# Performance work log

Hardware: AMD Instinct MI355X
Metric: run time of the kernel (lower is better)

## Reference

```python
import jax, jax.numpy as jnp
import numpy as np

NUM_HEADS = 12


def setup_inputs() -> dict:
    key = jax.random.key(0)
    ks = jax.random.split(key, 6)
    B, H, W, C = 8, 32, 32, 768
    hd = C // NUM_HEADS
    n = lambda k, shp, sc: jax.random.normal(k, shp, dtype=jnp.float32) * sc
    return {
        "x": n(ks[0], (B, H, W, C), 1.0),
        "qkv_w": n(ks[1], (3 * C, C), 0.02),
        "qkv_b": jnp.zeros((3 * C,), jnp.float32),
        "proj_w": n(ks[2], (C, C), 0.02),
        "proj_b": jnp.zeros((C,), jnp.float32),
        "rel_pos_h": n(ks[3], (2 * H - 1, hd), 0.02),
        "rel_pos_w": n(ks[4], (2 * W - 1, hd), 0.02),
    }


def reference(x, qkv_w, qkv_b, proj_w, proj_b, rel_pos_h, rel_pos_w):
    B, H, W, C = x.shape
    nH = NUM_HEADS
    hd = C // nH
    scale = hd ** -0.5
    # qkv projection (torch Linear convention: y = x @ W.T + b)
    qkv = x.reshape(B, H * W, C) @ qkv_w.T + qkv_b              # (B, HW, 3C)
    qkv = qkv.reshape(B, H * W, 3, nH, hd).transpose(2, 0, 3, 1, 4)
    qkv = qkv.reshape(3, B * nH, H * W, hd)
    q, k, v = qkv[0], qkv[1], qkv[2]
    attn = jnp.einsum('bqd,bkd->bqk', q * scale, k)             # (B*nH, HW, HW)
    # decomposed relative position bias (q_size == k_size, so no interpolation)
    coords_h = jnp.arange(H)[:, None] - jnp.arange(H)[None, :] + (H - 1)
    coords_w = jnp.arange(W)[:, None] - jnp.arange(W)[None, :] + (W - 1)
    Rh = rel_pos_h[coords_h]                                    # (H, H, hd)
    Rw = rel_pos_w[coords_w]                                    # (W, W, hd)
    r_q = q.reshape(B * nH, H, W, hd)
    rel_h = jnp.einsum('bhwc,hkc->bhwk', r_q, Rh)               # (B*nH, H, W, H)
    rel_w = jnp.einsum('bhwc,wkc->bhwk', r_q, Rw)               # (B*nH, H, W, W)
    attn = (attn.reshape(B * nH, H, W, H, W)
            + rel_h[..., :, None] + rel_w[..., None, :]).reshape(B * nH, H * W, H * W)
    attn = jax.nn.softmax(attn, axis=-1)
    out = attn @ v                                              # (B*nH, HW, hd)
    out = out.reshape(B, nH, H, W, hd).transpose(0, 2, 3, 1, 4).reshape(B, H, W, C)
    return out @ proj_w.T + proj_b
```

## Files before the change

### kernel.cpp

```cpp
#include <hip/hip_runtime.h>

using u16 = unsigned short;
using u32 = unsigned int;
typedef __attribute__((ext_vector_type(8))) short bf16x8;
typedef __attribute__((ext_vector_type(4))) float f32x4;

__device__ __forceinline__ float bf2f(u32 h) {
  union { u32 u; float f; } c; c.u = h << 16; return c.f;
}
__device__ __forceinline__ u16 f2bf(float f) {
  union { float f; u32 u; } c; c.f = f;
  u32 u = c.u;
  u32 r = (u + 0x7FFFu + ((u >> 16) & 1u)) >> 16;
  return (u16)r;
}

#define GLD16(gsrc, ldst)                                                      \
  __builtin_amdgcn_global_load_lds(                                            \
      (const __attribute__((address_space(1))) unsigned int*)(gsrc),           \
      (__attribute__((address_space(3))) unsigned int*)(ldst), 16, 0, 0)

__device__ __forceinline__ int kappa(int ss) {
  return (ss & 0x23) | ((ss & 0x10) >> 2) | ((ss & 0x0C) << 1);
}

__device__ __forceinline__ bf16x8 onehot8(int c) {
  union { u32 w[4]; bf16x8 v; } u;
  u32 hv = (c & 1) ? 0x3F800000u : 0x3F80u;
#pragma unroll
  for (int k = 0; k < 4; ++k) u.w[k] = ((c >> 1) == k) ? hv : 0u;
  return u.v;
}

__global__ void cvt_kernel(const float* __restrict__ src, u16* __restrict__ dst, int n) {
  int i = (blockIdx.x * blockDim.x + threadIdx.x) * 4;
  if (i < n) {
    float4 v = *(const float4*)(src + i);
    ushort4 o;
    o.x = f2bf(v.x); o.y = f2bf(v.y); o.z = f2bf(v.z); o.w = f2bf(v.w);
    *(ushort4*)(dst + i) = o;
  }
}

__global__ void tbl_kernel(const float* __restrict__ rph, const float* __restrict__ rpw,
                           u16* __restrict__ tbl) {
  int i = blockIdx.x * 256 + threadIdx.x;
  int row = i >> 6, d = i & 63;
  float v = 0.f;
  if (row < 63) v = rph[row * 64 + d];
  else if (row >= 64 && row < 127) v = rpw[(row - 64) * 64 + d];
  tbl[i] = f2bf(v * 8.0f);
}

__global__ __launch_bounds__(256, 2) void pgemm_kernel(
    const u16* __restrict__ A, const u16* __restrict__ tbl, u16* __restrict__ Q2) {
  __shared__ u16 As[128 * 64];
  __shared__ u16 Bs[128 * 64];
  const int tid = threadIdx.x;
  const int lane = tid & 63, wave = tid >> 6;
  const int lr = lane & 15, lg = lane >> 4;
  const int m0 = blockIdx.x * 128;
  const int wm = (wave >> 1) * 64, wn = (wave & 1) * 64;

#pragma unroll
  for (int i = 0; i < 4; ++i) {
    int c = tid + i * 256;
    int row = c >> 3, pp = c & 7;
    int pl = pp ^ (row & 7);
    GLD16(A + (size_t)(m0 + row) * 128 + pl * 8, &As[c * 8]);
    GLD16(tbl + row * 64 + pl * 8, &Bs[c * 8]);
  }
  __syncthreads();

  bf16x8 a[4][2], b[4][2];
#pragma unroll
  for (int m = 0; m < 4; ++m) {
    int row = wm + m * 16 + lr;
#pragma unroll
    for (int kf = 0; kf < 2; ++kf)
      a[m][kf] = *(const bf16x8*)&As[(row * 64 + kf * 32 + lg * 8) ^ ((row & 7) << 3)];
  }
#pragma unroll
  for (int n = 0; n < 4; ++n) {
    int row = wn + n * 16 + lr;
#pragma unroll
    for (int kf = 0; kf < 2; ++kf)
      b[n][kf] = *(const bf16x8*)&Bs[(row * 64 + kf * 32 + lg * 8) ^ ((row & 7) << 3)];
  }

  f32x4 acc[4][4] = {};
#pragma unroll
  for (int kf = 0; kf < 2; ++kf)
#pragma unroll
    for (int m = 0; m < 4; ++m)
#pragma unroll
      for (int n = 0; n < 4; ++n)
        acc[m][n] = __builtin_amdgcn_mfma_f32_16x16x32_bf16(a[m][kf], b[n][kf], acc[m][n], 0, 0, 0);

#pragma unroll
  for (int m = 0; m < 4; ++m)
#pragma unroll
    for (int n = 0; n < 4; ++n) {
      const int col = wn + n * 16 + lr;
#pragma unroll
      for (int r = 0; r < 4; ++r) {
        const int g = m0 + wm + m * 16 + lg * 4 + r;
        const int s = g & 1023;
        const int hq = s >> 5, w = s & 31;
        u16 hv = f2bf(acc[m][n][r]);
        if (col < 64) {
          int kh = hq + 31 - col;
          if ((unsigned)kh < 32u) Q2[(size_t)g * 128 + 96 + kh] = hv;
        } else {
          int kw = w + 95 - col;
          if ((unsigned)kw < 32u) Q2[(size_t)g * 128 + 64 + kw] = hv;
        }
      }
    }
}

template <int MODE>
__global__ __launch_bounds__(512, 2) void gemm128(
    const u16* __restrict__ A, const u16* __restrict__ B,
    const float* __restrict__ bias, u16* __restrict__ oq, u16* __restrict__ ok,
    u16* __restrict__ ovt, float* __restrict__ ofp) {
  __shared__ u16 As[2][128 * 64];
  __shared__ u16 Bs[2][128 * 64];
  const int tid = threadIdx.x;
  const int lane = tid & 63, wave = tid >> 6;
  const int lr = lane & 15, lg = lane >> 4;

  const int nbx = (MODE == 0) ? 18 : 6;
  const int nwg = nbx * 64;
  int id = blockIdx.y * nbx + blockIdx.x;
  int nid = (id & 7) * (nwg >> 3) + (id >> 3);
  const int m0 = (nid / nbx) * 128, n0 = (nid % nbx) * 128;
  const int wm = (wave >> 2) * 64, wn = (wave & 3) * 32;

  f32x4 acc[4][2] = {};

  const u16* ap[2];
  const u16* bp[2];
#pragma unroll
  for (int i = 0; i < 2; ++i) {
    int c = tid + i * 512;
    int row = c >> 3, pp = c & 7;
    int pl = pp ^ (row & 7);
    if constexpr (MODE == 0) {
      ap[i] = A + (size_t)(m0 + row) * 768 + pl * 8;
    } else {
      int g = m0 + row;
      ap[i] = A + ((size_t)((g >> 10) * 12) << 16) + (g & 1023) * 64 + pl * 8;
    }
    bp[i] = B + (size_t)(n0 + row) * 768 + pl * 8;
  }
  constexpr int dA = (MODE == 0) ? 64 : 65536;

  auto stage = [&](int bi) {
#pragma unroll
    for (int i = 0; i < 2; ++i) {
      int c = tid + i * 512;
      GLD16(ap[i], &As[bi][c * 8]);
      GLD16(bp[i], &Bs[bi][c * 8]);
      ap[i] += dA;
      bp[i] += 64;
    }
  };

  stage(0);
#pragma unroll 1
  for (int t = 0; t < 12; ++t) {
    const int cur = t & 1;
    if (t < 11) {
      stage(cur ^ 1);
      asm volatile("s_waitcnt vmcnt(4)" ::: "memory");
    } else {
      asm volatile("s_waitcnt vmcnt(0)" ::: "memory");
    }
    __builtin_amdgcn_sched_barrier(0);
    __builtin_amdgcn_s_barrier();
    __builtin_amdgcn_sched_barrier(0);

    bf16x8 a[4][2], b[2][2];
#pragma unroll
    for (int m = 0; m < 4; ++m) {
      int row = wm + m * 16 + lr;
#pragma unroll
      for (int kf = 0; kf < 2; ++kf)
        a[m][kf] = *(const bf16x8*)&As[cur][(row * 64 + kf * 32 + lg * 8) ^ ((row & 7) << 3)];
    }
#pragma unroll
    for (int n = 0; n < 2; ++n) {
      int row = wn + n * 16 + lr;
#pragma unroll
      for (int kf = 0; kf < 2; ++kf)
        b[n][kf] = *(const bf16x8*)&Bs[cur][(row * 64 + kf * 32 + lg * 8) ^ ((row & 7) << 3)];
    }
    __builtin_amdgcn_s_setprio(1);
#pragma unroll
    for (int kf = 0; kf < 2; ++kf)
#pragma unroll
      for (int m = 0; m < 4; ++m)
#pragma unroll
        for (int n = 0; n < 2; ++n)
          acc[m][n] = __builtin_amdgcn_mfma_f32_16x16x32_bf16(a[m][kf], b[n][kf], acc[m][n], 0, 0, 0);
    __builtin_amdgcn_s_setprio(0);

    __builtin_amdgcn_sched_barrier(0);
    __builtin_amdgcn_s_barrier();
    __builtin_amdgcn_sched_barrier(0);
  }

#pragma unroll
  for (int m = 0; m < 4; ++m) {
    const int grow0 = m0 + wm + m * 16 + lg * 4;
#pragma unroll
    for (int n = 0; n < 2; ++n) {
      const int gcol = n0 + wn + n * 16 + lr;
      const float bv = bias[gcol];
      if constexpr (MODE == 0) {
        int which = (gcol >= 1536) ? 2 : (gcol >= 768 ? 1 : 0);
        int rem = gcol - which * 768;
        int bh = (grow0 >> 10) * 12 + (rem >> 6);
        if (which == 2) {
          int s0 = grow0 & 1023;
          int colb = (s0 & ~63) | kappa(s0 & 63);
          ushort4 pk;
          pk.x = f2bf(acc[m][n][0] + bv);
          pk.y = f2bf(acc[m][n][1] + bv);
          pk.z = f2bf(acc[m][n][2] + bv);
          pk.w = f2bf(acc[m][n][3] + bv);
          *(ushort4*)&ovt[((size_t)bh << 16) + (size_t)(rem & 63) * 1024 + colb] = pk;
        } else if (which == 0) {
#pragma unroll
          for (int r = 0; r < 4; ++r) {
            int s = (grow0 & 1023) + r;
            oq[((size_t)bh << 17) + s * 128 + (rem & 63)] =
                f2bf((acc[m][n][r] + bv) * 0.18033688f);
          }
        } else {
#pragma unroll
          for (int r = 0; r < 4; ++r) {
            int s = (grow0 & 1023) + r;
            ok[((size_t)bh << 16) + s * 64 + (rem & 63)] = f2bf(acc[m][n][r] + bv);
          }
        }
      } else {
#pragma unroll
        for (int r = 0; r < 4; ++r)
          ofp[(size_t)(grow0 + r) * 768 + gcol] = acc[m][n][r] + bv;
      }
    }
  }
}

__global__ __launch_bounds__(256, 2) void attn_kernel(
    const u16* __restrict__ qb, const u16* __restrict__ kb,
    const u16* __restrict__ vtb, u16* __restrict__ ao) {
  __shared__ u16 Ks[2][4096];
  __shared__ u16 Vs[2][4096];

  const int tid = threadIdx.x;
  const int lane = tid & 63, wave = tid >> 6;
  const int lr = lane & 15, lg = lane >> 4;
  const int bh = blockIdx.x;
  const int q0 = blockIdx.y * 128 + wave * 32;
  const size_t hb2 = (size_t)bh << 17;
  const size_t hbv = (size_t)bh << 16;

  bf16x8 qf[2][4];
#pragma unroll
  for (int m = 0; m < 2; ++m)
#pragma unroll
    for (int kf = 0; kf < 4; ++kf)
      qf[m][kf] = *(const bf16x8*)(qb + hb2 + (size_t)(q0 + m * 16 + lr) * 128 + kf * 32 + lg * 8);

  bf16x8 kwf[2];
#pragma unroll
  for (int h = 0; h < 2; ++h) kwf[h] = onehot8(h * 16 + lr - lg * 8);

  float lsum[2] = {};
  f32x4 acco[2][4] = {};

  const u16* kp[2];
  const u16* vp[2];
#pragma unroll
  for (int i = 0; i < 2; ++i) {
    int c = tid + i * 256;
    int row = c >> 3, pp = c & 7;
    int pl = pp ^ (row & 7);
    kp[i] = kb + hbv + (size_t)row * 64 + pl * 8;
    vp[i] = vtb + hbv + (size_t)row * 1024 + pl * 8;
  }

  auto stage = [&](int bi) {
#pragma unroll
    for (int i = 0; i < 2; ++i) {
      int c = tid + i * 256;
      GLD16(kp[i], &Ks[bi][c * 8]);
      GLD16(vp[i], &Vs[bi][c * 8]);
      kp[i] += 4096;
      vp[i] += 64;
    }
  };

  stage(0);

#pragma unroll 1
  for (int t = 0; t < 16; ++t) {
    const int cur = t & 1;
    if (t < 15) {
      stage(cur ^ 1);
      asm volatile("s_waitcnt vmcnt(4)" ::: "memory");
    } else {
      asm volatile("s_waitcnt vmcnt(0)" ::: "memory");
    }
    __builtin_amdgcn_sched_barrier(0);
    __builtin_amdgcn_s_barrier();
    __builtin_amdgcn_sched_barrier(0);

    bf16x8 khf[2];
#pragma unroll
    for (int h = 0; h < 2; ++h) khf[h] = onehot8(2 * t + h - lg * 8);

    f32x4 sac[2][4] = {};
    __builtin_amdgcn_s_setprio(1);
#pragma unroll
    for (int kf = 0; kf < 2; ++kf) {
#pragma unroll
      for (int f = 0; f < 4; ++f) {
        int row = f * 16 + lr;
        bf16x8 kv = *(const bf16x8*)&Ks[cur][(row * 64 + kf * 32 + lg * 8) ^ ((row & 7) << 3)];
#pragma unroll
        for (int m = 0; m < 2; ++m)
          sac[m][f] = __builtin_amdgcn_mfma_f32_16x16x32_bf16(kv, qf[m][kf], sac[m][f], 0, 0, 0);
      }
    }
#pragma unroll
    for (int f = 0; f < 4; ++f)
#pragma unroll
      for (int m = 0; m < 2; ++m)
        sac[m][f] = __builtin_amdgcn_mfma_f32_16x16x32_bf16(kwf[f & 1], qf[m][2], sac[m][f], 0, 0, 0);
#pragma unroll
    for (int f = 0; f < 4; ++f)
#pragma unroll
      for (int m = 0; m < 2; ++m)
        sac[m][f] = __builtin_amdgcn_mfma_f32_16x16x32_bf16(khf[f >> 1], qf[m][3], sac[m][f], 0, 0, 0);
    __builtin_amdgcn_s_setprio(0);

    bf16x8 paf[2][2];
#pragma unroll
    for (int m = 0; m < 2; ++m) {
      union { u32 w[4]; bf16x8 v; } wa, wb;
#pragma unroll
      for (int f = 0; f < 4; ++f) {
        float p0 = __builtin_amdgcn_exp2f(sac[m][f][0]);
        float p1 = __builtin_amdgcn_exp2f(sac[m][f][1]);
        float p2 = __builtin_amdgcn_exp2f(sac[m][f][2]);
        float p3 = __builtin_amdgcn_exp2f(sac[m][f][3]);
        lsum[m] += (p0 + p1) + (p2 + p3);
        u32 w0, w1;
        asm("v_cvt_pk_bf16_f32 %0, %1, %2" : "=v"(w0) : "v"(p0), "v"(p1));
        asm("v_cvt_pk_bf16_f32 %0, %1, %2" : "=v"(w1) : "v"(p2), "v"(p3));
        if (f < 2) { wa.w[f * 2] = w0; wa.w[f * 2 + 1] = w1; }
        else       { wb.w[(f - 2) * 2] = w0; wb.w[(f - 2) * 2 + 1] = w1; }
      }
      paf[m][0] = wa.v;
      paf[m][1] = wb.v;
    }

    __builtin_amdgcn_s_setprio(1);
#pragma unroll
    for (int kf = 0; kf < 2; ++kf) {
#pragma unroll
      for (int fd = 0; fd < 4; ++fd) {
        int drow = fd * 16 + lr;
        bf16x8 vv = *(const bf16x8*)&Vs[cur][(drow * 64 + kf * 32 + lg * 8) ^ ((drow & 7) << 3)];
#pragma unroll
        for (int m = 0; m < 2; ++m)
          acco[m][fd] = __builtin_amdgcn_mfma_f32_16x16x32_bf16(paf[m][kf], vv, acco[m][fd], 0, 0, 0);
      }
    }
    __builtin_amdgcn_s_setprio(0);

    __builtin_amdgcn_sched_barrier(0);
    __builtin_amdgcn_s_barrier();
    __builtin_amdgcn_sched_barrier(0);
  }

#pragma unroll
  for (int m = 0; m < 2; ++m) {
    float s = lsum[m];
    s += __shfl_xor(s, 16);
    s += __shfl_xor(s, 32);
    float inv = 1.0f / s;
#pragma unroll
    for (int r = 0; r < 4; ++r) {
      int src = (lane & 48) + ((lane & 48) >> 2) + r;
      float invr = __shfl(inv, src);
      int gq = q0 + m * 16 + lg * 4 + r;
#pragma unroll
      for (int fd = 0; fd < 4; ++fd)
        ao[hbv + (size_t)gq * 64 + fd * 16 + lr] = f2bf(acco[m][fd][r] * invr);
    }
  }
}

extern "C" void kernel_launch(void* const* d_in, const int* in_sizes, int n_in,
                              void* d_out, int out_size, void* d_ws, size_t ws_size,
                              hipStream_t stream) {
  const float* x = (const float*)d_in[0];
  const float* qkv_w = (const float*)d_in[1];
  const float* qkv_b = (const float*)d_in[2];
  const float* proj_w = (const float*)d_in[3];
  const float* proj_b = (const float*)d_in[4];
  const float* rel_pos_h = (const float*)d_in[5];
  const float* rel_pos_w = (const float*)d_in[6];
  float* out = (float*)d_out;

  char* ws = (char*)d_ws;
  u16* x_bf = (u16*)(ws + 0);
  u16* qkvw_bf = (u16*)(ws + 12582912);
  u16* projw_bf = (u16*)(ws + 16121856);
  u16* qbuf2 = (u16*)(ws + 17301504);
  u16* kbuf = (u16*)(ws + 42467328);
  u16* vtbuf = (u16*)(ws + 55050240);
  u16* tbl = (u16*)(ws + 67633152);
  u16* aobuf = x_bf;

  cvt_kernel<<<6144, 256, 0, stream>>>(x, x_bf, 6291456);
  cvt_kernel<<<1728, 256, 0, stream>>>(qkv_w, qkvw_bf, 1769472);
  cvt_kernel<<<576, 256, 0, stream>>>(proj_w, projw_bf, 589824);
  tbl_kernel<<<32, 256, 0, stream>>>(rel_pos_h, rel_pos_w, tbl);

  gemm128<0><<<dim3(18, 64), 512, 0, stream>>>(x_bf, qkvw_bf, qkv_b, qbuf2, kbuf, vtbuf, nullptr);

  pgemm_kernel<<<768, 256, 0, stream>>>(qbuf2, tbl, qbuf2);

  attn_kernel<<<dim3(96, 8), 256, 0, stream>>>(qbuf2, kbuf, vtbuf, aobuf);

  gemm128<1><<<dim3(6, 64), 512, 0, stream>>>(aobuf, projw_bf, proj_b, nullptr, nullptr, nullptr, out);
}
```

Before: 124.6 us.

## Fuse prep conversions, hoist loop-invariant rel-w bias MFMA, widen pgemm tiles

The three fp32-to-bf16 conversion launches and the table build are merged into one prep kernel, removing three launches. The pgemm kernel now processes two 128-row A tiles per block and reuses the table fragments, halving its grid. In the attention kernel, the width relative-bias MFMA does not depend on the key tile, so it is computed once before the loop and used to seed the score accumulators, saving 8 MFMAs per iteration. The GEMM hoists its swizzled LDS offsets out of the k loop, at the cost of more live registers.

```diff
diff --git a/kernel.cpp b/kernel.cpp
--- a/kernel.cpp
+++ b/kernel.cpp
@@ -32,34 +32,46 @@
   return u.v;
 }
 
-__global__ void cvt_kernel(const float* __restrict__ src, u16* __restrict__ dst, int n) {
-  int i = (blockIdx.x * blockDim.x + threadIdx.x) * 4;
-  if (i < n) {
-    float4 v = *(const float4*)(src + i);
+__global__ void prep_kernel(const float* __restrict__ x, const float* __restrict__ qw,
+                            const float* __restrict__ pw, const float* __restrict__ rph,
+                            const float* __restrict__ rpw, u16* __restrict__ xb,
+                            u16* __restrict__ qwb, u16* __restrict__ pwb,
+                            u16* __restrict__ tbl) {
+  int i = blockIdx.x * 256 + threadIdx.x;
+  const float* src;
+  u16* dst;
+  int j;
+  if (i < 1572864) { src = x; dst = xb; j = i; }
+  else if (i < 2015232) { src = qw; dst = qwb; j = i - 1572864; }
+  else if (i < 2162688) { src = pw; dst = pwb; j = i - 2015232; }
+  else {
+    int b = (i - 2162688) * 4;
     ushort4 o;
-    o.x = f2bf(v.x); o.y = f2bf(v.y); o.z = f2bf(v.z); o.w = f2bf(v.w);
-    *(ushort4*)(dst + i) = o;
-  }
-}
-
-__global__ void tbl_kernel(const float* __restrict__ rph, const float* __restrict__ rpw,
-                           u16* __restrict__ tbl) {
-  int i = blockIdx.x * 256 + threadIdx.x;
-  int row = i >> 6, d = i & 63;
-  float v = 0.f;
-  if (row < 63) v = rph[row * 64 + d];
-  else if (row >= 64 && row < 127) v = rpw[(row - 64) * 64 + d];
-  tbl[i] = f2bf(v * 8.0f);
+#pragma unroll
+    for (int k = 0; k < 4; ++k) {
+      int idx = b + k, row = idx >> 6, d = idx & 63;
+      float v = 0.f;
+      if (row < 63) v = rph[row * 64 + d];
+      else if (row >= 64 && row < 127) v = rpw[(row - 64) * 64 + d];
+      ((u16*)&o)[k] = f2bf(v * 8.0f);
+    }
+    *(ushort4*)&tbl[b] = o;
+    return;
+  }
+  float4 v = *(const float4*)(src + j * 4);
+  ushort4 o;
+  o.x = f2bf(v.x); o.y = f2bf(v.y); o.z = f2bf(v.z); o.w = f2bf(v.w);
+  *(ushort4*)(dst + j * 4) = o;
 }
 
 __global__ __launch_bounds__(256, 2) void pgemm_kernel(
     const u16* __restrict__ A, const u16* __restrict__ tbl, u16* __restrict__ Q2) {
-  __shared__ u16 As[128 * 64];
+  __shared__ u16 As[2][128 * 64];
   __shared__ u16 Bs[128 * 64];
   const int tid = threadIdx.x;
   const int lane = tid & 63, wave = tid >> 6;
   const int lr = lane & 15, lg = lane >> 4;
-  const int m0 = blockIdx.x * 128;
+  const int m0 = blockIdx.x * 256;
   const int wm = (wave >> 1) * 64, wn = (wave & 1) * 64;
 
 #pragma unroll
@@ -67,19 +79,14 @@
     int c = tid + i * 256;
     int row = c >> 3, pp = c & 7;
     int pl = pp ^ (row & 7);
-    GLD16(A + (size_t)(m0 + row) * 128 + pl * 8, &As[c * 8]);
     GLD16(tbl + row * 64 + pl * 8, &Bs[c * 8]);
+#pragma unroll
+    for (int tt = 0; tt < 2; ++tt)
+      GLD16(A + (size_t)(m0 + tt * 128 + row) * 128 + pl * 8, &As[tt][c * 8]);
   }
   __syncthreads();
 
-  bf16x8 a[4][2], b[4][2];
-#pragma unroll
-  for (int m = 0; m < 4; ++m) {
-    int row = wm + m * 16 + lr;
-#pragma unroll
-    for (int kf = 0; kf < 2; ++kf)
-      a[m][kf] = *(const bf16x8*)&As[(row * 64 + kf * 32 + lg * 8) ^ ((row & 7) << 3)];
-  }
+  bf16x8 b[4][2];
 #pragma unroll
   for (int n = 0; n < 4; ++n) {
     int row = wn + n * 16 + lr;
@@ -88,35 +95,46 @@
       b[n][kf] = *(const bf16x8*)&Bs[(row * 64 + kf * 32 + lg * 8) ^ ((row & 7) << 3)];
   }
 
-  f32x4 acc[4][4] = {};
-#pragma unroll
-  for (int kf = 0; kf < 2; ++kf)
+#pragma unroll
+  for (int tt = 0; tt < 2; ++tt) {
+    bf16x8 a[4][2];
+#pragma unroll
+    for (int m = 0; m < 4; ++m) {
+      int row = wm + m * 16 + lr;
+#pragma unroll
+      for (int kf = 0; kf < 2; ++kf)
+        a[m][kf] = *(const bf16x8*)&As[tt][(row * 64 + kf * 32 + lg * 8) ^ ((row & 7) << 3)];
+    }
+    f32x4 acc[4][4] = {};
+#pragma unroll
+    for (int kf = 0; kf < 2; ++kf)
+#pragma unroll
+      for (int m = 0; m < 4; ++m)
+#pragma unroll
+        for (int n = 0; n < 4; ++n)
+          acc[m][n] = __builtin_amdgcn_mfma_f32_16x16x32_bf16(a[m][kf], b[n][kf], acc[m][n], 0, 0, 0);
+
 #pragma unroll
     for (int m = 0; m < 4; ++m)
 #pragma unroll
-      for (int n = 0; n < 4; ++n)
-        acc[m][n] = __builtin_amdgcn_mfma_f32_16x16x32_bf16(a[m][kf], b[n][kf], acc[m][n], 0, 0, 0);
-
-#pragma unroll
-  for (int m = 0; m < 4; ++m)
-#pragma unroll
-    for (int n = 0; n < 4; ++n) {
-      const int col = wn + n * 16 + lr;
-#pragma unroll
-      for (int r = 0; r < 4; ++r) {
-        const int g = m0 + wm + m * 16 + lg * 4 + r;
-        const int s = g & 1023;
-        const int hq = s >> 5, w = s & 31;
-        u16 hv = f2bf(acc[m][n][r]);
-        if (col < 64) {
-          int kh = hq + 31 - col;
-          if ((unsigned)kh < 32u) Q2[(size_t)g * 128 + 96 + kh] = hv;
-        } else {
-          int kw = w + 95 - col;
-          if ((unsigned)kw < 32u) Q2[(size_t)g * 128 + 64 + kw] = hv;
+      for (int n = 0; n < 4; ++n) {
+        const int col = wn + n * 16 + lr;
+#pragma unroll
+        for (int r = 0; r < 4; ++r) {
+          const int g = m0 + tt * 128 + wm + m * 16 + lg * 4 + r;
+          const int s = g & 1023;
+          const int hq = s >> 5, w = s & 31;
+          u16 hv = f2bf(acc[m][n][r]);
+          if (col < 64) {
+            int kh = hq + 31 - col;
+            if ((unsigned)kh < 32u) Q2[(size_t)g * 128 + 96 + kh] = hv;
+          } else {
+            int kw = w + 95 - col;
+            if ((unsigned)kw < 32u) Q2[(size_t)g * 128 + 64 + kw] = hv;
+          }
         }
       }
-    }
+  }
 }
 
 template <int MODE>
@@ -139,6 +157,22 @@
 
   f32x4 acc[4][2] = {};
 
+  int aoff[4][2], boff[2][2];
+#pragma unroll
+  for (int m = 0; m < 4; ++m) {
+    int row = wm + m * 16 + lr;
+#pragma unroll
+    for (int kf = 0; kf < 2; ++kf)
+      aoff[m][kf] = (row * 64 + kf * 32 + lg * 8) ^ ((row & 7) << 3);
+  }
+#pragma unroll
+  for (int n = 0; n < 2; ++n) {
+    int row = wn + n * 16 + lr;
+#pragma unroll
+    for (int kf = 0; kf < 2; ++kf)
+      boff[n][kf] = (row * 64 + kf * 32 + lg * 8) ^ ((row & 7) << 3);
+  }
+
   const u16* ap[2];
   const u16* bp[2];
 #pragma unroll
@@ -183,19 +217,15 @@
 
     bf16x8 a[4][2], b[2][2];
 #pragma unroll
-    for (int m = 0; m < 4; ++m) {
-      int row = wm + m * 16 + lr;
+    for (int m = 0; m < 4; ++m)
 #pragma unroll
       for (int kf = 0; kf < 2; ++kf)
-        a[m][kf] = *(const bf16x8*)&As[cur][(row * 64 + kf * 32 + lg * 8) ^ ((row & 7) << 3)];
-    }
-#pragma unroll
-    for (int n = 0; n < 2; ++n) {
-      int row = wn + n * 16 + lr;
+        a[m][kf] = *(const bf16x8*)&As[cur][aoff[m][kf]];
+#pragma unroll
+    for (int n = 0; n < 2; ++n)
 #pragma unroll
       for (int kf = 0; kf < 2; ++kf)
-        b[n][kf] = *(const bf16x8*)&Bs[cur][(row * 64 + kf * 32 + lg * 8) ^ ((row & 7) << 3)];
-    }
+        b[n][kf] = *(const bf16x8*)&Bs[cur][boff[n][kf]];
     __builtin_amdgcn_s_setprio(1);
 #pragma unroll
     for (int kf = 0; kf < 2; ++kf)
@@ -275,9 +305,14 @@
     for (int kf = 0; kf < 4; ++kf)
       qf[m][kf] = *(const bf16x8*)(qb + hb2 + (size_t)(q0 + m * 16 + lr) * 128 + kf * 32 + lg * 8);
 
-  bf16x8 kwf[2];
-#pragma unroll
-  for (int h = 0; h < 2; ++h) kwf[h] = onehot8(h * 16 + lr - lg * 8);
+  f32x4 sacW[2][2] = {};
+#pragma unroll
+  for (int h = 0; h < 2; ++h) {
+    bf16x8 kwf = onehot8(h * 16 + lr - lg * 8);
+#pragma unroll
+    for (int m = 0; m < 2; ++m)
+      sacW[m][h] = __builtin_amdgcn_mfma_f32_16x16x32_bf16(kwf, qf[m][2], sacW[m][h], 0, 0, 0);
+  }
 
   float lsum[2] = {};
   f32x4 acco[2][4] = {};
@@ -323,7 +358,11 @@
 #pragma unroll
     for (int h = 0; h < 2; ++h) khf[h] = onehot8(2 * t + h - lg * 8);
 
-    f32x4 sac[2][4] = {};
+    f32x4 sac[2][4];
+#pragma unroll
+    for (int m = 0; m < 2; ++m)
+#pragma unroll
+      for (int f = 0; f < 4; ++f) sac[m][f] = sacW[m][f & 1];
     __builtin_amdgcn_s_setprio(1);
 #pragma unroll
     for (int kf = 0; kf < 2; ++kf) {
@@ -336,11 +375,6 @@
           sac[m][f] = __builtin_amdgcn_mfma_f32_16x16x32_bf16(kv, qf[m][kf], sac[m][f], 0, 0, 0);
       }
     }
-#pragma unroll
-    for (int f = 0; f < 4; ++f)
-#pragma unroll
-      for (int m = 0; m < 2; ++m)
-        sac[m][f] = __builtin_amdgcn_mfma_f32_16x16x32_bf16(kwf[f & 1], qf[m][2], sac[m][f], 0, 0, 0);
 #pragma unroll
     for (int f = 0; f < 4; ++f)
 #pragma unroll
@@ -428,14 +462,12 @@
   u16* tbl = (u16*)(ws + 67633152);
   u16* aobuf = x_bf;
 
-  cvt_kernel<<<6144, 256, 0, stream>>>(x, x_bf, 6291456);
-  cvt_kernel<<<1728, 256, 0, stream>>>(qkv_w, qkvw_bf, 1769472);
-  cvt_kernel<<<576, 256, 0, stream>>>(proj_w, projw_bf, 589824);
-  tbl_kernel<<<32, 256, 0, stream>>>(rel_pos_h, rel_pos_w, tbl);
+  prep_kernel<<<8456, 256, 0, stream>>>(x, qkv_w, proj_w, rel_pos_h, rel_pos_w,
+                                        x_bf, qkvw_bf, projw_bf, tbl);
 
   gemm128<0><<<dim3(18, 64), 512, 0, stream>>>(x_bf, qkvw_bf, qkv_b, qbuf2, kbuf, vtbuf, nullptr);
 
-  pgemm_kernel<<<768, 256, 0, stream>>>(qbuf2, tbl, qbuf2);
+  pgemm_kernel<<<384, 256, 0, stream>>>(qbuf2, tbl, qbuf2);
 
   attn_kernel<<<dim3(96, 8), 256, 0, stream>>>(qbuf2, kbuf, vtbuf, aobuf);
 
```

Result: faster. 120.5 us (-3.3%).
